# Kernel optimization log

Hardware: AMD Instinct MI355X
Metric: run time of the kernel (lower is better)

## Reference

```python
import jax, jax.numpy as jnp
import numpy as np

D = 128
B = 512
N = 512
MAX_HOPS = 3


def _masked_softmax(v, mask, axis):
    m = jnp.max(v, axis=axis, keepdims=True)
    e = jnp.exp(v - m) * mask
    s = jnp.sum(e, axis=axis, keepdims=True) + 1e-5
    return e / s


def _l2_norm(x):
    # torch renorm(p=2, dim=0, maxnorm=1e-12).mul(1e12): rows with norm>maxnorm -> x/norm,
    # rows with norm<=maxnorm stay unchanged then *1e12
    maxnorm = 1e-12
    norm = jnp.sqrt(jnp.sum(x * x, axis=1, keepdims=True))
    safe = jnp.maximum(norm, maxnorm)
    return jnp.where(norm > maxnorm, x / safe, x * (1.0 / maxnorm))


def setup_inputs() -> dict:
    key = jax.random.key(0)
    ks = jax.random.split(key, 12)
    xavier = lambda k, shp: jax.random.uniform(k, shp, jnp.float32, -1.0, 1.0) * np.sqrt(6.0 / (shp[0] + shp[1]))
    return {
        "e1_embeded": jax.random.normal(ks[0], (B, D), jnp.float32),
        "rel_embeded": jax.random.normal(ks[1], (B, D), jnp.float32),
        "nei_embeded_key": jax.random.normal(ks[2], (B, N, D), jnp.float32),
        "nei_embeded_value": jax.random.normal(ks[3], (B, N, D), jnp.float32),
        "nei_mask": jax.random.randint(ks[4], (B, N), 0, 2, jnp.int32),
        "Wk": xavier(ks[5], (D, D)),
        "Wv": xavier(ks[6], (D, D)),
        "W_lin": xavier(ks[7], (D, D)),
        "b_lin": jnp.zeros((D,), jnp.float32),
        "W_att": xavier(ks[8], (3 * D, D)),
        "b_att": jnp.zeros((D,), jnp.float32),
        "dim": 2,
    }


def reference(e1_embeded, rel_embeded, nei_embeded_key, nei_embeded_value, nei_mask,
              Wk, Wv, W_lin, b_lin, W_att, b_att, dim):
    mask = nei_mask.astype(jnp.float32)  # [B,N]
    fk = jnp.einsum('bnd,de->bne', nei_embeded_key * mask[..., None], Wk)   # [B,N,D]
    fv = jnp.einsum('bnd,de->bne', nei_embeded_value * mask[..., None], Wv)  # [B,N,D]
    n = fk.shape[1]
    rel_b = jnp.broadcast_to(rel_embeded[:, None, :], fk.shape)
    u = e1_embeded
    for _ in range(MAX_HOPS):
        u_batch = jax.nn.leaky_relu(u @ W_lin + b_lin)                      # [B,D]
        ent_b = jnp.broadcast_to(u[:, None, :], fk.shape)
        m = jnp.concatenate([fk, ent_b, rel_b], axis=2)                      # [B,N,3D]
        att = jnp.sum(jax.nn.leaky_relu(jnp.einsum('bnk,kd->bnd', m, W_att) + b_att), axis=2)  # [B,N]
        p = _masked_softmax(att, mask, axis=1)
        o = jnp.sum(fv * p[..., None], axis=1)                               # [B,D]
        u = _l2_norm(u_batch + o)
    return u
```

## Files before the change

kernel.cpp:

```cpp
#include <hip/hip_runtime.h>

#define D 128
#define NN 512
#define BB 512

typedef __attribute__((ext_vector_type(8))) short short8;
typedef __attribute__((ext_vector_type(4))) float f32x4;

__device__ __forceinline__ unsigned int fbits(float f) {
  union { float f; unsigned int u; } v; v.f = f; return v.u;
}
__device__ __forceinline__ float ubits(unsigned int u) {
  union { unsigned int u; float f; } v; v.u = u; return v.f;
}
__device__ __forceinline__ unsigned short f2bf(float f) {
  unsigned int x = fbits(f);
  return (unsigned short)((x + 0x7fffu + ((x >> 16) & 1u)) >> 16);
}
__device__ __forceinline__ float h2f(unsigned short u) {
  _Float16 h; __builtin_memcpy(&h, &u, 2); return (float)h;
}
__device__ __forceinline__ unsigned short f2h(float f) {
  _Float16 h = (_Float16)f; unsigned short u; __builtin_memcpy(&u, &h, 2); return u;
}
__device__ __forceinline__ float lrelu(float x) { return x > 0.f ? x : 0.01f * x; }

__device__ __forceinline__ int fragidx(int k, int n) {
  return ((((n >> 4) * 4 + (k >> 5)) * 64 + ((k >> 3) & 3) * 16 + (n & 15)) << 3) + (k & 7);
}

__global__ __launch_bounds__(256) void prep_kernel(
    const float* __restrict__ Wk, const float* __restrict__ Watt,
    const float* __restrict__ batt, const float* __restrict__ rel,
    unsigned short* __restrict__ WhF, unsigned short* __restrict__ WlF,
    float* __restrict__ c3) {
  __shared__ float rowS[D];
  __shared__ float psum[2][D];
  const int blk = blockIdx.x;
  const int t = threadIdx.x;
  const float* src = (blk < D) ? (Wk + blk * D) : (rel + (blk - D) * D);
  const float* W   = (blk < D) ? Watt : (Watt + 2 * D * D);
  if (t < D) rowS[t] = src[t];
  __syncthreads();
  const int d = t & 127, half = t >> 7;
  const float* Wp = W + (half * 64) * D + d;
  float a = 0.f;
  #pragma unroll 8
  for (int k = 0; k < 64; ++k) a += rowS[half * 64 + k] * Wp[k * D];
  psum[half][d] = a;
  __syncthreads();
  if (t < D) {
    const float w = psum[0][t] + psum[1][t];
    if (blk < D) {
      const unsigned int ub = fbits(w);
      const int idx = fragidx(blk, t);
      WhF[idx] = (unsigned short)(ub >> 16);
      WlF[idx] = f2bf(w - ubits(ub & 0xFFFF0000u));
    } else {
      c3[(blk - D) * D + t] = w + batt[t];
    }
  }
}

__global__ __launch_bounds__(256) void gemm_g1_kernel(
    const float* __restrict__ key, const int* __restrict__ mask,
    const unsigned short* __restrict__ WhF, const unsigned short* __restrict__ WlF,
    unsigned short* __restrict__ g1h) {
  __shared__ __align__(16) unsigned short whlds[16384];
  __shared__ __align__(16) unsigned short wllds[16384];
  const int t = threadIdx.x;
  #pragma unroll
  for (int i = 0; i < 8; ++i) {
    const int unit = t + i * 256;
    *reinterpret_cast<uint4*>(&whlds[unit * 8]) = *reinterpret_cast<const uint4*>(WhF + unit * 8);
    *reinterpret_cast<uint4*>(&wllds[unit * 8]) = *reinterpret_cast<const uint4*>(WlF + unit * 8);
  }
  __syncthreads();
  const int wave = t >> 6, lane = t & 63;
  const int q = lane >> 4, l15 = lane & 15;
  const short8 zero8 = {0, 0, 0, 0, 0, 0, 0, 0};
  const int ntiles = (BB * NN) / 64;
  for (int tile = blockIdx.x; tile < ntiles; tile += gridDim.x) {
    const long rowbase = (long)tile * 64 + wave * 16;
    const long r = rowbase + l15;
    const int mk = mask[r];
    short8 ah[4], al[4];
    if (mk) {
      #pragma unroll
      for (int kt = 0; kt < 4; ++kt) {
        const float* kp = key + r * D + kt * 32 + q * 8;
        float xs[8];
        *reinterpret_cast<float4*>(&xs[0]) = *reinterpret_cast<const float4*>(kp);
        *reinterpret_cast<float4*>(&xs[4]) = *reinterpret_cast<const float4*>(kp + 4);
        union { unsigned int u[4]; short8 v; } cvh, cvl;
        #pragma unroll
        for (int p2 = 0; p2 < 4; ++p2) {
          const float a = xs[2 * p2], b = xs[2 * p2 + 1];
          const unsigned int ua = fbits(a), ub = fbits(b);
          cvh.u[p2] = (ua >> 16) | (ub & 0xFFFF0000u);
          const float ra = a - ubits(ua & 0xFFFF0000u);
          const float rb = b - ubits(ub & 0xFFFF0000u);
          cvl.u[p2] = (unsigned int)f2bf(ra) | ((unsigned int)f2bf(rb) << 16);
        }
        ah[kt] = cvh.v; al[kt] = cvl.v;
      }
    } else {
      #pragma unroll
      for (int kt = 0; kt < 4; ++kt) { ah[kt] = zero8; al[kt] = zero8; }
    }
    f32x4 acc[8];
    #pragma unroll
    for (int c = 0; c < 8; ++c) acc[c] = (f32x4){0.f, 0.f, 0.f, 0.f};
    #pragma unroll
    for (int kt = 0; kt < 4; ++kt) {
      #pragma unroll
      for (int c = 0; c < 8; ++c) {
        const short8 bh = *reinterpret_cast<const short8*>(&whlds[((c * 4 + kt) * 64 + lane) * 8]);
        const short8 bl = *reinterpret_cast<const short8*>(&wllds[((c * 4 + kt) * 64 + lane) * 8]);
        acc[c] = __builtin_amdgcn_mfma_f32_16x16x32_bf16(ah[kt], bh, acc[c], 0, 0, 0);
        acc[c] = __builtin_amdgcn_mfma_f32_16x16x32_bf16(al[kt], bh, acc[c], 0, 0, 0);
        acc[c] = __builtin_amdgcn_mfma_f32_16x16x32_bf16(ah[kt], bl, acc[c], 0, 0, 0);
      }
    }
    const int4 mr4 = *reinterpret_cast<const int4*>(mask + rowbase + q * 4);
    const int mrr[4] = {mr4.x, mr4.y, mr4.z, mr4.w};
    #pragma unroll
    for (int c = 0; c < 8; ++c) {
      #pragma unroll
      for (int reg = 0; reg < 4; ++reg) {
        if (mrr[reg]) {
          const long row = rowbase + q * 4 + reg;
          g1h[row * D + c * 16 + l15] = f2h(acc[c][reg]);
        }
      }
    }
  }
}

__global__ __launch_bounds__(512, 4) void hops_kernel(
    const float* __restrict__ e1, const int* __restrict__ mask,
    const float* __restrict__ value, const unsigned short* __restrict__ g1h,
    const float* __restrict__ Wlin, const float* __restrict__ blin,
    const float* __restrict__ Watt, const float* __restrict__ Wv,
    const float* __restrict__ c3, float* __restrict__ out) {
  __shared__ float uS[D], cS[D], ubS[D], opS[D];
  __shared__ float attS[NN];
  __shared__ float part[4][D];
  __shared__ float oscr[8][D];
  __shared__ float redA[8], redB[8];
  __shared__ int idxS[NN];
  __shared__ int redI[8];
  __shared__ int padRowS;
  const int b = blockIdx.x;
  const int t = threadIdx.x;
  const int wv = t >> 6, lane = t & 63;
  const int grp = t >> 4, l = t & 15, d0 = (t & 15) * 8;
  const long base = (long)b * NN * D;
  const int* mb = mask + b * NN;
  if (t < D) uS[t] = e1[b * D + t];
  const int myMask = mb[t];
  {
    const unsigned long long bal = __ballot(myMask != 0);
    const int lanePre = __popcll(bal & ((1ULL << lane) - 1ULL));
    if (lane == 0) redI[wv] = __popcll(bal);
    if (!myMask) padRowS = t;
    __syncthreads();
    int wbase = 0, cnt = 0;
    #pragma unroll
    for (int w2 = 0; w2 < 8; ++w2) {
      const int c = redI[w2];
      if (w2 < wv) wbase += c;
      cnt += c;
    }
    if (myMask) idxS[wbase + lanePre] = t;
    const int cntPad = (cnt + 127) & ~127;
    __syncthreads();
    for (int i = cnt + t; i < cntPad; i += 512) idxS[i] = padRowS;
    redI[0] = cntPad >> 7;
    __syncthreads();
  }
  const int nb = redI[0];
  for (int hop = 0; hop < 3; ++hop) {
    {
      const int d = t & 127, role = t >> 7;
      const float* W = (role < 2) ? (Watt + D * D) : Wlin;
      const int k0 = (role & 1) * 64;
      const float* Wp = W + k0 * D + d;
      float a = 0.f;
      #pragma unroll 8
      for (int k = 0; k < 64; ++k) a += uS[k0 + k] * Wp[k * D];
      part[role][d] = a;
    }
    __syncthreads();
    if (t < D) cS[t] = part[0][t] + part[1][t] + c3[b * D + t];
    else if (t < 2 * D) { const int d = t - D; ubS[d] = lrelu(part[2][d] + part[3][d] + blin[d]); }
    __syncthreads();
    if (t < 128) {
      float v = lrelu(cS[t]);
      #pragma unroll
      for (int off = 32; off > 0; off >>= 1) v += __shfl_xor(v, off, 64);
      if (lane == 0) redB[wv] = v;
    }
    {
      float creg[8];
      #pragma unroll
      for (int j = 0; j < 8; ++j) creg[j] = cS[d0 + j];
      for (int ii = 0; ii < nb; ++ii) {
        int ns[4]; uint4 g[4];
        #pragma unroll
        for (int j2 = 0; j2 < 4; ++j2) ns[j2] = idxS[ii * 128 + j2 * 32 + grp];
        #pragma unroll
        for (int j2 = 0; j2 < 4; ++j2)
          g[j2] = *reinterpret_cast<const uint4*>(g1h + base + (long)ns[j2] * D + d0);
        #pragma unroll
        for (int j2 = 0; j2 < 4; ++j2) {
          const unsigned short* e = reinterpret_cast<const unsigned short*>(&g[j2]);
          float s = 0.f;
          #pragma unroll
          for (int j = 0; j < 8; ++j) s += lrelu(h2f(e[j]) + creg[j]);
          #pragma unroll
          for (int off = 8; off > 0; off >>= 1) s += __shfl_xor(s, off, 16);
          if (l == 0) attS[ns[j2]] = s;
        }
      }
    }
    __syncthreads();
    {
      const float av = myMask ? attS[t] : (redB[0] + redB[1]);
      float m = av;
      #pragma unroll
      for (int off = 32; off > 0; off >>= 1) m = fmaxf(m, __shfl_xor(m, off, 64));
      if (lane == 0) redA[wv] = m;
      __syncthreads();
      m = redA[0];
      #pragma unroll
      for (int w2 = 1; w2 < 8; ++w2) m = fmaxf(m, redA[w2]);
      const float e0 = __expf(av - m) * (myMask ? 1.f : 0.f);
      float ss = e0;
      #pragma unroll
      for (int off = 32; off > 0; off >>= 1) ss += __shfl_xor(ss, off, 64);
      if (lane == 0) redB[wv] = ss;
      __syncthreads();
      float s = 1e-5f;
      #pragma unroll
      for (int w2 = 0; w2 < 8; ++w2) s += redB[w2];
      attS[t] = e0 / s;
    }
    __syncthreads();
    {
      float acc8[8];
      #pragma unroll
      for (int j = 0; j < 8; ++j) acc8[j] = 0.f;
      for (int ii = 0; ii < nb; ++ii) {
        int ns[4]; float4 va[4], vb[4];
        #pragma unroll
        for (int j2 = 0; j2 < 4; ++j2) ns[j2] = idxS[ii * 128 + j2 * 32 + grp];
        #pragma unroll
        for (int j2 = 0; j2 < 4; ++j2) {
          const float* vp = value + base + (long)ns[j2] * D + d0;
          va[j2] = *reinterpret_cast<const float4*>(vp);
          vb[j2] = *reinterpret_cast<const float4*>(vp + 4);
        }
        #pragma unroll
        for (int j2 = 0; j2 < 4; ++j2) {
          const float p = attS[ns[j2]];
          acc8[0] += p * va[j2].x; acc8[1] += p * va[j2].y;
          acc8[2] += p * va[j2].z; acc8[3] += p * va[j2].w;
          acc8[4] += p * vb[j2].x; acc8[5] += p * vb[j2].y;
          acc8[6] += p * vb[j2].z; acc8[7] += p * vb[j2].w;
        }
      }
      #pragma unroll
      for (int j = 0; j < 8; ++j) {
        acc8[j] += __shfl_xor(acc8[j], 16, 64);
        acc8[j] += __shfl_xor(acc8[j], 32, 64);
      }
      if (lane < 16) {
        #pragma unroll
        for (int j = 0; j < 8; ++j) oscr[wv][lane * 8 + j] = acc8[j];
      }
    }
    __syncthreads();
    if (t < D) {
      float s = 0.f;
      #pragma unroll
      for (int w2 = 0; w2 < 8; ++w2) s += oscr[w2][t];
      opS[t] = s;
    }
    __syncthreads();
    {
      const int d = t & 127, role = t >> 7;
      const int k0 = role * 32;
      const float* Wp = Wv + k0 * D + d;
      float a = 0.f;
      #pragma unroll 8
      for (int k = 0; k < 32; ++k) a += opS[k0 + k] * Wp[k * D];
      part[role][d] = a;
    }
    __syncthreads();
    {
      float un = 0.f, sq = 0.f;
      if (t < D) {
        un = ubS[t] + part[0][t] + part[1][t] + part[2][t] + part[3][t];
        sq = un * un;
      }
      #pragma unroll
      for (int off = 32; off > 0; off >>= 1) sq += __shfl_xor(sq, off, 64);
      if (lane == 0) redA[wv] = sq;
      __syncthreads();
      float ns = 0.f;
      #pragma unroll
      for (int w2 = 0; w2 < 8; ++w2) ns += redA[w2];
      const float norm = sqrtf(ns);
      const float inv = (norm > 1e-12f) ? (1.f / norm) : 1e12f;
      if (t < D) uS[t] = un * inv;
    }
    __syncthreads();
  }
  if (t < D) out[b * D + t] = uS[t];
}

extern "C" void kernel_launch(void* const* d_in, const int* in_sizes, int n_in,
                              void* d_out, int out_size, void* d_ws, size_t ws_size,
                              hipStream_t stream) {
  const float* e1   = (const float*)d_in[0];
  const float* rel  = (const float*)d_in[1];
  const float* key  = (const float*)d_in[2];
  const float* val  = (const float*)d_in[3];
  const int*   mask = (const int*)d_in[4];
  const float* Wk   = (const float*)d_in[5];
  const float* Wv   = (const float*)d_in[6];
  const float* Wlin = (const float*)d_in[7];
  const float* blin = (const float*)d_in[8];
  const float* Watt = (const float*)d_in[9];
  const float* batt = (const float*)d_in[10];
  float* out = (float*)d_out;

  char* ws = (char*)d_ws;
  unsigned short* WhF = (unsigned short*)ws;
  unsigned short* WlF = (unsigned short*)(ws + 32 * 1024);
  float*          c3  = (float*)(ws + 64 * 1024);
  unsigned short* g1h = (unsigned short*)(ws + 512 * 1024);

  prep_kernel<<<D + BB, 256, 0, stream>>>(Wk, Watt, batt, rel, WhF, WlF, c3);
  gemm_g1_kernel<<<1024, 256, 0, stream>>>(key, mask, WhF, WlF, g1h);
  hops_kernel<<<BB, 512, 0, stream>>>(e1, mask, val, g1h, Wlin, blin, Watt, Wv, c3, out);
}
```

Measured before the change: 380.5 us.

## Split g1 GEMM output columns across block pairs and stream key conversion per k-tile

Each block now covers half of the 128 output columns (selected by block index parity), so it loads half the weight fragments into LDS and keeps four accumulators instead of eight. The grid is doubled to 2048 to keep the same row coverage. Key loading and bf16 split conversion move inside the k loop, which cuts register pressure and should allow higher occupancy. In exchange every key row is read and converted twice, once per column half, which doubles global key traffic, and masked rows are now loaded instead of skipped.

```diff
diff --git a/kernel.cpp b/kernel.cpp
--- a/kernel.cpp
+++ b/kernel.cpp
@@ -66,71 +66,66 @@
     const float* __restrict__ key, const int* __restrict__ mask,
     const unsigned short* __restrict__ WhF, const unsigned short* __restrict__ WlF,
     unsigned short* __restrict__ g1h) {
-  __shared__ __align__(16) unsigned short whlds[16384];
-  __shared__ __align__(16) unsigned short wllds[16384];
+  __shared__ __align__(16) unsigned short whlds[8192];
+  __shared__ __align__(16) unsigned short wllds[8192];
   const int t = threadIdx.x;
+  const int ch = blockIdx.x & 1;
+  const unsigned short* Wh = WhF + ch * 8192;
+  const unsigned short* Wl = WlF + ch * 8192;
   #pragma unroll
-  for (int i = 0; i < 8; ++i) {
+  for (int i = 0; i < 4; ++i) {
     const int unit = t + i * 256;
-    *reinterpret_cast<uint4*>(&whlds[unit * 8]) = *reinterpret_cast<const uint4*>(WhF + unit * 8);
-    *reinterpret_cast<uint4*>(&wllds[unit * 8]) = *reinterpret_cast<const uint4*>(WlF + unit * 8);
+    *reinterpret_cast<uint4*>(&whlds[unit * 8]) = *reinterpret_cast<const uint4*>(Wh + unit * 8);
+    *reinterpret_cast<uint4*>(&wllds[unit * 8]) = *reinterpret_cast<const uint4*>(Wl + unit * 8);
   }
   __syncthreads();
   const int wave = t >> 6, lane = t & 63;
   const int q = lane >> 4, l15 = lane & 15;
-  const short8 zero8 = {0, 0, 0, 0, 0, 0, 0, 0};
-  const int ntiles = (BB * NN) / 64;
-  for (int tile = blockIdx.x; tile < ntiles; tile += gridDim.x) {
-    const long rowbase = (long)tile * 64 + wave * 16;
+  const int nrt = (BB * NN) / 64;
+  const int rstride = gridDim.x >> 1;
+  for (int rt = blockIdx.x >> 1; rt < nrt; rt += rstride) {
+    const long rowbase = (long)rt * 64 + wave * 16;
     const long r = rowbase + l15;
     const int mk = mask[r];
-    short8 ah[4], al[4];
-    if (mk) {
-      #pragma unroll
-      for (int kt = 0; kt < 4; ++kt) {
-        const float* kp = key + r * D + kt * 32 + q * 8;
-        float xs[8];
-        *reinterpret_cast<float4*>(&xs[0]) = *reinterpret_cast<const float4*>(kp);
-        *reinterpret_cast<float4*>(&xs[4]) = *reinterpret_cast<const float4*>(kp + 4);
-        union { unsigned int u[4]; short8 v; } cvh, cvl;
-        #pragma unroll
-        for (int p2 = 0; p2 < 4; ++p2) {
-          const float a = xs[2 * p2], b = xs[2 * p2 + 1];
-          const unsigned int ua = fbits(a), ub = fbits(b);
-          cvh.u[p2] = (ua >> 16) | (ub & 0xFFFF0000u);
-          const float ra = a - ubits(ua & 0xFFFF0000u);
-          const float rb = b - ubits(ub & 0xFFFF0000u);
-          cvl.u[p2] = (unsigned int)f2bf(ra) | ((unsigned int)f2bf(rb) << 16);
-        }
-        ah[kt] = cvh.v; al[kt] = cvl.v;
-      }
-    } else {
-      #pragma unroll
-      for (int kt = 0; kt < 4; ++kt) { ah[kt] = zero8; al[kt] = zero8; }
-    }
-    f32x4 acc[8];
+    f32x4 acc[4];
     #pragma unroll
-    for (int c = 0; c < 8; ++c) acc[c] = (f32x4){0.f, 0.f, 0.f, 0.f};
+    for (int c = 0; c < 4; ++c) acc[c] = (f32x4){0.f, 0.f, 0.f, 0.f};
     #pragma unroll
     for (int kt = 0; kt < 4; ++kt) {
-      #pragma unroll
-      for (int c = 0; c < 8; ++c) {
+      const float* kp = key + r * D + kt * 32 + q * 8;
+      float xs[8];
+      *reinterpret_cast<float4*>(&xs[0]) = *reinterpret_cast<const float4*>(kp);
+      *reinterpret_cast<float4*>(&xs[4]) = *reinterpret_cast<const float4*>(kp + 4);
+      union { unsigned int u[4]; short8 v; } cvh, cvl;
+      #pragma unroll
+      for (int p2 = 0; p2 < 4; ++p2) {
+        float a = xs[2 * p2], b = xs[2 * p2 + 1];
+        if (!mk) { a = 0.f; b = 0.f; }
+        const unsigned int ua = fbits(a), ub = fbits(b);
+        cvh.u[p2] = (ua >> 16) | (ub & 0xFFFF0000u);
+        const float ra = a - ubits(ua & 0xFFFF0000u);
+        const float rb = b - ubits(ub & 0xFFFF0000u);
+        cvl.u[p2] = (unsigned int)f2bf(ra) | ((unsigned int)f2bf(rb) << 16);
+      }
+      const short8 ah = cvh.v, al = cvl.v;
+      #pragma unroll
+      for (int c = 0; c < 4; ++c) {
         const short8 bh = *reinterpret_cast<const short8*>(&whlds[((c * 4 + kt) * 64 + lane) * 8]);
         const short8 bl = *reinterpret_cast<const short8*>(&wllds[((c * 4 + kt) * 64 + lane) * 8]);
-        acc[c] = __builtin_amdgcn_mfma_f32_16x16x32_bf16(ah[kt], bh, acc[c], 0, 0, 0);
-        acc[c] = __builtin_amdgcn_mfma_f32_16x16x32_bf16(al[kt], bh, acc[c], 0, 0, 0);
-        acc[c] = __builtin_amdgcn_mfma_f32_16x16x32_bf16(ah[kt], bl, acc[c], 0, 0, 0);
+        acc[c] = __builtin_amdgcn_mfma_f32_16x16x32_bf16(ah, bh, acc[c], 0, 0, 0);
+        acc[c] = __builtin_amdgcn_mfma_f32_16x16x32_bf16(al, bh, acc[c], 0, 0, 0);
+        acc[c] = __builtin_amdgcn_mfma_f32_16x16x32_bf16(ah, bl, acc[c], 0, 0, 0);
       }
     }
     const int4 mr4 = *reinterpret_cast<const int4*>(mask + rowbase + q * 4);
     const int mrr[4] = {mr4.x, mr4.y, mr4.z, mr4.w};
     #pragma unroll
-    for (int c = 0; c < 8; ++c) {
+    for (int c = 0; c < 4; ++c) {
       #pragma unroll
       for (int reg = 0; reg < 4; ++reg) {
         if (mrr[reg]) {
           const long row = rowbase + q * 4 + reg;
-          g1h[row * D + c * 16 + l15] = f2h(acc[c][reg]);
+          g1h[row * D + ch * 64 + c * 16 + l15] = f2h(acc[c][reg]);
         }
       }
     }
@@ -343,6 +338,6 @@
   unsigned short* g1h = (unsigned short*)(ws + 512 * 1024);
 
   prep_kernel<<<D + BB, 256, 0, stream>>>(Wk, Watt, batt, rel, WhF, WlF, c3);
-  gemm_g1_kernel<<<1024, 256, 0, stream>>>(key, mask, WhF, WlF, g1h);
+  gemm_g1_kernel<<<2048, 256, 0, stream>>>(key, mask, WhF, WlF, g1h);
   hops_kernel<<<BB, 512, 0, stream>>>(e1, mask, val, g1h, Wlin, blin, Watt, Wv, c3, out);
 }
```

Result: faster. 356.2 us (-6.4%).
